# Kernel optimization log

Measured on AMD Instinct MI355X. Metric: run time of the kernel, lower is better.

Reference implementation:

```python
import jax, jax.numpy as jnp
import numpy as np

N_POINTS = 2_000_000
GRID = (128, 128, 128)
N_COMP = 3


def _bspline_weights(u):
    # cubic B-spline basis, returns tuple of 4 arrays shaped like u
    u2 = u * u
    u3 = u2 * u
    w0 = (1.0 - u) ** 3 / 6.0
    w1 = (3.0 * u3 - 6.0 * u2 + 4.0) / 6.0
    w2 = (-3.0 * u3 + 3.0 * u2 + 3.0 * u + 1.0) / 6.0
    w3 = u3 / 6.0
    return (w0, w1, w2, w3)


def setup_inputs() -> dict:
    key = jax.random.key(0)
    kx, ky, kz, kp = jax.random.split(key, 4)
    # query points uniform in the supported domain [-1, 1]
    x = jax.random.uniform(kx, (N_POINTS,), jnp.float32, -1.0, 1.0)
    y = jax.random.uniform(ky, (N_POINTS,), jnp.float32, -1.0, 1.0)
    z = jax.random.uniform(kz, (N_POINTS,), jnp.float32, -1.0, 1.0)
    phi_x = jax.random.normal(kp, (*GRID, N_COMP), jnp.float32)
    return {"x": x, "y": y, "z": z, "phi_x": phi_x}


def reference(x, y, z, phi_x):
    # BSplineField3d.vectorized_displacement with support_outside=True,
    # default support_range=None -> spacing = 2/(n-3), origin = -1 - spacing.
    nx, ny, nz, _ = phi_x.shape
    dx = 2.0 / (nx - 3)
    dy = 2.0 / (ny - 3)
    dz = 2.0 / (nz - 3)
    ox, oy, oz = -1.0 - dx, -1.0 - dy, -1.0 - dz

    u = (x - ox - dx) / dx
    v = (y - oy - dy) / dy
    w = (z - oz - dz) / dz
    ix = jnp.floor(u).astype(jnp.int32)
    iy = jnp.floor(v).astype(jnp.int32)
    iz = jnp.floor(w).astype(jnp.int32)
    u = u - ix
    v = v - iy
    w = w - iz

    wu = _bspline_weights(u)
    wv = _bspline_weights(v)
    ww = _bspline_weights(w)

    T = jnp.zeros((x.shape[0], phi_x.shape[-1]), dtype=x.dtype)
    # 64 fixed taps: gather from control grid at clamped indices, MAC.
    for l in range(4):
        ixl = jnp.clip(ix + l, 0, nx - 1)
        for m in range(4):
            iym = jnp.clip(iy + m, 0, ny - 1)
            wum = wu[l] * wv[m]
            for n in range(4):
                izn = jnp.clip(iz + n, 0, nz - 1)
                coef = wum * ww[n]  # [N]
                T = T + coef[:, None] * phi_x[ixl, iym, izn]  # gather [N, C]
    return T
```

## Files before the change

kernel.cpp:

```cpp
#include <hip/hip_runtime.h>


#define NBINS 4096
#define NBLK  256
#define BRICK 1331

__device__ __forceinline__ void bspline_w(float u, float& w0, float& w1,
                                          float& w2, float& w3) {
    const float u2 = u * u;
    const float u3 = u2 * u;
    const float t  = 1.0f - u;
    w0 = t * t * t * (1.0f / 6.0f);
    w1 = (3.0f * u3 - 6.0f * u2 + 4.0f) * (1.0f / 6.0f);
    w2 = (-3.0f * u3 + 3.0f * u2 + 3.0f * u + 1.0f) * (1.0f / 6.0f);
    w3 = u3 * (1.0f / 6.0f);
}

__device__ __forceinline__ void cell_ids(float x, float y, float z,
                                         int& ix, int& iy, int& iz) {
    const float dx = 2.0f / 125.0f;
    const float ox = -1.0f - dx;
    const float u = (x - ox - dx) / dx;
    const float v = (y - ox - dx) / dx;
    const float w = (z - ox - dx) / dx;
    ix = (int)floorf(u);
    iy = (int)floorf(v);
    iz = (int)floorf(w);
}

__device__ __forceinline__ int point_bin(float x, float y, float z) {
    int ix, iy, iz;
    cell_ids(x, y, z, ix, iy, iz);
    const int bx = min(max(ix, 0), 127) >> 3;
    const int by = min(max(iy, 0), 127) >> 3;
    const int bz = min(max(iz, 0), 127) >> 3;
    return (bx << 8) | (by << 4) | bz;
}

__global__ __launch_bounds__(256) void hist_kernel(
    const float* __restrict__ xs, const float* __restrict__ ys,
    const float* __restrict__ zs, unsigned* __restrict__ hist,
    int n, int chunk) {
    __shared__ unsigned h[NBINS];
    for (int j = threadIdx.x; j < NBINS; j += 256) h[j] = 0;
    __syncthreads();
    const int b = blockIdx.x;
    const int lo = b * chunk;
    const int hi = min(n, lo + chunk);
    for (int i = lo + threadIdx.x; i < hi; i += 256) {
        atomicAdd(&h[point_bin(xs[i], ys[i], zs[i])], 1u);
    }
    __syncthreads();
    for (int j = threadIdx.x; j < NBINS; j += 256) hist[b * NBINS + j] = h[j];
}

__global__ __launch_bounds__(256) void totals_kernel(
    const unsigned* __restrict__ hist, unsigned* __restrict__ total) {
    const int j = blockIdx.x * 256 + threadIdx.x;
    unsigned s = 0;
    for (int b = 0; b < NBLK; ++b) s += hist[b * NBINS + j];
    total[j] = s;
}

__global__ __launch_bounds__(1024) void scan_kernel(
    const unsigned* __restrict__ total, unsigned* __restrict__ binbase) {
    __shared__ unsigned sdata[1024];
    const int t = threadIdx.x;
    const unsigned v0 = total[4 * t + 0];
    const unsigned v1 = total[4 * t + 1];
    const unsigned v2 = total[4 * t + 2];
    const unsigned v3 = total[4 * t + 3];
    sdata[t] = v0 + v1 + v2 + v3;
    __syncthreads();
    for (int off = 1; off < 1024; off <<= 1) {
        unsigned x = (t >= off) ? sdata[t - off] : 0u;
        __syncthreads();
        sdata[t] += x;
        __syncthreads();
    }
    const unsigned ex = (t > 0) ? sdata[t - 1] : 0u;
    binbase[4 * t + 0] = ex;
    binbase[4 * t + 1] = ex + v0;
    binbase[4 * t + 2] = ex + v0 + v1;
    binbase[4 * t + 3] = ex + v0 + v1 + v2;
}

__global__ __launch_bounds__(256) void fixup_kernel(
    unsigned* __restrict__ hist, const unsigned* __restrict__ binbase) {
    const int j = blockIdx.x * 256 + threadIdx.x;
    unsigned run = binbase[j];
    for (int b = 0; b < NBLK; ++b) {
        const unsigned c = hist[b * NBINS + j];
        hist[b * NBINS + j] = run;
        run += c;
    }
}

__global__ __launch_bounds__(256) void scatter_kernel(
    const float* __restrict__ xs, const float* __restrict__ ys,
    const float* __restrict__ zs, const unsigned* __restrict__ hist,
    float4* __restrict__ rec, int n, int chunk) {
    __shared__ unsigned off[NBINS];
    const int b = blockIdx.x;
    for (int j = threadIdx.x; j < NBINS; j += 256) off[j] = hist[b * NBINS + j];
    __syncthreads();
    const int lo = b * chunk;
    const int hi = min(n, lo + chunk);
    for (int i = lo + threadIdx.x; i < hi; i += 256) {
        const float x = xs[i], y = ys[i], z = zs[i];
        const unsigned p = atomicAdd(&off[point_bin(x, y, z)], 1u);
        rec[p] = make_float4(x, y, z, __int_as_float(i));
    }
}

__global__ __launch_bounds__(256) void eval_kernel(
    const float4* __restrict__ rec, const unsigned* __restrict__ binbase,
    const unsigned* __restrict__ total, const float* __restrict__ phi,
    float* __restrict__ out) {
    const int bin = blockIdx.x;
    const unsigned cnt = total[bin];
    if (cnt == 0) return;
    const unsigned start = binbase[bin];

    const int gx0 = ((bin >> 8) & 15) << 3;
    const int gy0 = ((bin >> 4) & 15) << 3;
    const int gz0 = (bin & 15) << 3;

    __shared__ float4 brick[BRICK];
    for (int p = threadIdx.x; p < BRICK; p += 256) {
        const int lx = p / 121;
        const int r  = p - lx * 121;
        const int ly = r / 11;
        const int lz = r - ly * 11;
        const int gx = min(gx0 + lx, 127);
        const int gy = min(gy0 + ly, 127);
        const int gz = min(gz0 + lz, 127);
        const float* s = phi + (size_t)((gx * 128 + gy) * 128 + gz) * 3;
        brick[p] = make_float4(s[0], s[1], s[2], 0.0f);
    }
    __syncthreads();

    for (unsigned k = start + threadIdx.x; k < start + cnt; k += 256) {
        const float4 r4 = rec[k];
        const int idx = __float_as_int(r4.w);

        int ix, iy, iz;
        cell_ids(r4.x, r4.y, r4.z, ix, iy, iz);
        const float dx = 2.0f / 125.0f;
        const float ox = -1.0f - dx;
        float u = (r4.x - ox - dx) / dx - floorf((r4.x - ox - dx) / dx);
        float v = (r4.y - ox - dx) / dx - floorf((r4.y - ox - dx) / dx);
        float w = (r4.z - ox - dx) / dx - floorf((r4.z - ox - dx) / dx);

        float wu[4], wv[4], wz[4];
        bspline_w(u, wu[0], wu[1], wu[2], wu[3]);
        bspline_w(v, wv[0], wv[1], wv[2], wv[3]);
        bspline_w(w, wz[0], wz[1], wz[2], wz[3]);

        int izb = iz < 0 ? 0 : iz;
        const bool sh = izb > 124;
        if (sh) izb = 124;
        const float zw0 = sh ? 0.0f : wz[0];
        const float zw1 = sh ? wz[0] : wz[1];
        const float zw2 = sh ? wz[1] : wz[2];
        const float zw3 = sh ? (wz[2] + wz[3]) : wz[3];
        const int lzb = izb - gz0;

        int lxi[4], lyi[4];
#pragma unroll
        for (int l = 0; l < 4; ++l) {
            lxi[l] = min(max(ix + l, 0), 127) - gx0;
            lyi[l] = min(max(iy + l, 0), 127) - gy0;
        }

        float acc0 = 0.0f, acc1 = 0.0f, acc2 = 0.0f;
#pragma unroll
        for (int l = 0; l < 4; ++l) {
            const int rowx = lxi[l] * 11;
#pragma unroll
            for (int m = 0; m < 4; ++m) {
                const float4* p0 = &brick[(rowx + lyi[m]) * 11 + lzb];
                const float wm = wu[l] * wv[m];
                const float c0 = wm * zw0;
                const float c1 = wm * zw1;
                const float c2 = wm * zw2;
                const float c3 = wm * zw3;
                const float4 a = p0[0];
                const float4 b = p0[1];
                const float4 c = p0[2];
                const float d = c3;
                const float4 e = p0[3];
                acc0 = fmaf(c0, a.x, acc0);
                acc1 = fmaf(c0, a.y, acc1);
                acc2 = fmaf(c0, a.z, acc2);
                acc0 = fmaf(c1, b.x, acc0);
                acc1 = fmaf(c1, b.y, acc1);
                acc2 = fmaf(c1, b.z, acc2);
                acc0 = fmaf(c2, c.x, acc0);
                acc1 = fmaf(c2, c.y, acc1);
                acc2 = fmaf(c2, c.z, acc2);
                acc0 = fmaf(d, e.x, acc0);
                acc1 = fmaf(d, e.y, acc1);
                acc2 = fmaf(d, e.z, acc2);
            }
        }
        float* o = out + 3 * (size_t)idx;
        o[0] = acc0;
        o[1] = acc1;
        o[2] = acc2;
    }
}

__global__ __launch_bounds__(256) void bspline3d_direct(
    const float* __restrict__ xs, const float* __restrict__ ys,
    const float* __restrict__ zs, const float* __restrict__ phi,
    float* __restrict__ out, int n) {
    const int i = blockIdx.x * blockDim.x + threadIdx.x;
    if (i >= n) return;
    const float dx = 2.0f / 125.0f;
    const float ox = -1.0f - dx;
    float u = (xs[i] - ox - dx) / dx;
    float v = (ys[i] - ox - dx) / dx;
    float w = (zs[i] - ox - dx) / dx;
    const float fu = floorf(u), fv = floorf(v), fw = floorf(w);
    const int ix = (int)fu, iy = (int)fv, iz = (int)fw;
    u -= fu; v -= fv; w -= fw;
    float wu[4], wv[4], wz[4];
    bspline_w(u, wu[0], wu[1], wu[2], wu[3]);
    bspline_w(v, wv[0], wv[1], wv[2], wv[3]);
    bspline_w(w, wz[0], wz[1], wz[2], wz[3]);
    int izb = iz < 0 ? 0 : iz;
    const bool sh = izb > 124;
    if (sh) izb = 124;
    const float zw0 = sh ? 0.0f : wz[0];
    const float zw1 = sh ? wz[0] : wz[1];
    const float zw2 = sh ? wz[1] : wz[2];
    const float zw3 = sh ? (wz[2] + wz[3]) : wz[3];
    int xi[4], yi[4];
#pragma unroll
    for (int l = 0; l < 4; ++l) {
        xi[l] = min(max(ix + l, 0), 127);
        yi[l] = min(max(iy + l, 0), 127);
    }
    const float* pz = phi + izb * 3;
    float acc0 = 0.0f, acc1 = 0.0f, acc2 = 0.0f;
#pragma unroll
    for (int l = 0; l < 4; ++l) {
        const int rowx = xi[l] << 7;
#pragma unroll
        for (int m = 0; m < 4; ++m) {
            const float* p = pz + (rowx + yi[m]) * 384;
            const float4 a = *reinterpret_cast<const float4*>(p);
            const float4 b = *reinterpret_cast<const float4*>(p + 4);
            const float4 c = *reinterpret_cast<const float4*>(p + 8);
            const float wm = wu[l] * wv[m];
            const float c0 = wm * zw0, c1 = wm * zw1, c2 = wm * zw2, c3 = wm * zw3;
            acc0 = fmaf(c0, a.x, acc0); acc1 = fmaf(c0, a.y, acc1); acc2 = fmaf(c0, a.z, acc2);
            acc0 = fmaf(c1, a.w, acc0); acc1 = fmaf(c1, b.x, acc1); acc2 = fmaf(c1, b.y, acc2);
            acc0 = fmaf(c2, b.z, acc0); acc1 = fmaf(c2, b.w, acc1); acc2 = fmaf(c2, c.x, acc2);
            acc0 = fmaf(c3, c.y, acc0); acc1 = fmaf(c3, c.z, acc1); acc2 = fmaf(c3, c.w, acc2);
        }
    }
    float* o = out + 3 * (size_t)i;
    o[0] = acc0; o[1] = acc1; o[2] = acc2;
}

extern "C" void kernel_launch(void* const* d_in, const int* in_sizes, int n_in,
                              void* d_out, int out_size, void* d_ws,
                              size_t ws_size, hipStream_t stream) {
    const float* xs  = (const float*)d_in[0];
    const float* ys  = (const float*)d_in[1];
    const float* zs  = (const float*)d_in[2];
    const float* phi = (const float*)d_in[3];
    float* out = (float*)d_out;
    const int n = in_sizes[0];

    const size_t hist_off = 0;
    const size_t total_off = hist_off + (size_t)NBLK * NBINS * 4;
    const size_t base_off  = total_off + NBINS * 4;
    const size_t rec_off   = base_off + NBINS * 4;
    const size_t need = rec_off + (size_t)n * 16;

    if (ws_size < need) {
        const int block = 256;
        bspline3d_direct<<<(n + block - 1) / block, block, 0, stream>>>(
            xs, ys, zs, phi, out, n);
        return;
    }

    unsigned* hist    = (unsigned*)((char*)d_ws + hist_off);
    unsigned* total   = (unsigned*)((char*)d_ws + total_off);
    unsigned* binbase = (unsigned*)((char*)d_ws + base_off);
    float4*   rec     = (float4*)((char*)d_ws + rec_off);

    const int chunk = (n + NBLK - 1) / NBLK;

    hist_kernel<<<NBLK, 256, 0, stream>>>(xs, ys, zs, hist, n, chunk);
    totals_kernel<<<NBINS / 256, 256, 0, stream>>>(hist, total);
    scan_kernel<<<1, 1024, 0, stream>>>(total, binbase);
    fixup_kernel<<<NBINS / 256, 256, 0, stream>>>(hist, binbase);
    scatter_kernel<<<NBLK, 256, 0, stream>>>(xs, ys, zs, hist, rec, n, chunk);
    eval_kernel<<<NBINS, 256, 0, stream>>>(rec, binbase, total, phi, out);
}
```

Before: 234.3 us.

## Simplify binning with global atomics and repack shared brick as per-component z-windows

```diff
diff --git a/kernel.cpp b/kernel.cpp
--- a/kernel.cpp
+++ b/kernel.cpp
@@ -2,8 +2,8 @@
 
 
 #define NBINS 4096
-#define NBLK  256
-#define BRICK 1331
+#define CUR_STRIDE 16
+#define NW (121 * 8 * 3)
 
 __device__ __forceinline__ void bspline_w(float u, float& w0, float& w1,
                                           float& w2, float& w3) {
@@ -20,12 +20,9 @@
                                          int& ix, int& iy, int& iz) {
     const float dx = 2.0f / 125.0f;
     const float ox = -1.0f - dx;
-    const float u = (x - ox - dx) / dx;
-    const float v = (y - ox - dx) / dx;
-    const float w = (z - ox - dx) / dx;
-    ix = (int)floorf(u);
-    iy = (int)floorf(v);
-    iz = (int)floorf(w);
+    ix = (int)floorf((x - ox - dx) / dx);
+    iy = (int)floorf((y - ox - dx) / dx);
+    iz = (int)floorf((z - ox - dx) / dx);
 }
 
 __device__ __forceinline__ int point_bin(float x, float y, float z) {
@@ -39,37 +36,27 @@
 
 __global__ __launch_bounds__(256) void hist_kernel(
     const float* __restrict__ xs, const float* __restrict__ ys,
-    const float* __restrict__ zs, unsigned* __restrict__ hist,
-    int n, int chunk) {
+    const float* __restrict__ zs, unsigned* __restrict__ hist, int n) {
     __shared__ unsigned h[NBINS];
     for (int j = threadIdx.x; j < NBINS; j += 256) h[j] = 0;
     __syncthreads();
-    const int b = blockIdx.x;
-    const int lo = b * chunk;
-    const int hi = min(n, lo + chunk);
-    for (int i = lo + threadIdx.x; i < hi; i += 256) {
+    const int stride = gridDim.x * 256;
+    for (int i = blockIdx.x * 256 + threadIdx.x; i < n; i += stride)
         atomicAdd(&h[point_bin(xs[i], ys[i], zs[i])], 1u);
-    }
-    __syncthreads();
-    for (int j = threadIdx.x; j < NBINS; j += 256) hist[b * NBINS + j] = h[j];
-}
-
-__global__ __launch_bounds__(256) void totals_kernel(
-    const unsigned* __restrict__ hist, unsigned* __restrict__ total) {
-    const int j = blockIdx.x * 256 + threadIdx.x;
-    unsigned s = 0;
-    for (int b = 0; b < NBLK; ++b) s += hist[b * NBINS + j];
-    total[j] = s;
+    __syncthreads();
+    for (int j = threadIdx.x; j < NBINS; j += 256)
+        if (h[j]) atomicAdd(&hist[j], h[j]);
 }
 
 __global__ __launch_bounds__(1024) void scan_kernel(
-    const unsigned* __restrict__ total, unsigned* __restrict__ binbase) {
+    const unsigned* __restrict__ hist, unsigned* __restrict__ binbase,
+    unsigned* __restrict__ cursor) {
     __shared__ unsigned sdata[1024];
     const int t = threadIdx.x;
-    const unsigned v0 = total[4 * t + 0];
-    const unsigned v1 = total[4 * t + 1];
-    const unsigned v2 = total[4 * t + 2];
-    const unsigned v3 = total[4 * t + 3];
+    const unsigned v0 = hist[4 * t + 0];
+    const unsigned v1 = hist[4 * t + 1];
+    const unsigned v2 = hist[4 * t + 2];
+    const unsigned v3 = hist[4 * t + 3];
     sdata[t] = v0 + v1 + v2 + v3;
     __syncthreads();
     for (int off = 1; off < 1024; off <<= 1) {
@@ -79,46 +66,39 @@
         __syncthreads();
     }
     const unsigned ex = (t > 0) ? sdata[t - 1] : 0u;
-    binbase[4 * t + 0] = ex;
-    binbase[4 * t + 1] = ex + v0;
-    binbase[4 * t + 2] = ex + v0 + v1;
-    binbase[4 * t + 3] = ex + v0 + v1 + v2;
-}
-
-__global__ __launch_bounds__(256) void fixup_kernel(
-    unsigned* __restrict__ hist, const unsigned* __restrict__ binbase) {
-    const int j = blockIdx.x * 256 + threadIdx.x;
-    unsigned run = binbase[j];
-    for (int b = 0; b < NBLK; ++b) {
-        const unsigned c = hist[b * NBINS + j];
-        hist[b * NBINS + j] = run;
-        run += c;
-    }
+    const unsigned b0 = ex;
+    const unsigned b1 = ex + v0;
+    const unsigned b2 = b1 + v1;
+    const unsigned b3 = b2 + v2;
+    binbase[4 * t + 0] = b0;
+    binbase[4 * t + 1] = b1;
+    binbase[4 * t + 2] = b2;
+    binbase[4 * t + 3] = b3;
+    cursor[(4 * t + 0) * CUR_STRIDE] = b0;
+    cursor[(4 * t + 1) * CUR_STRIDE] = b1;
+    cursor[(4 * t + 2) * CUR_STRIDE] = b2;
+    cursor[(4 * t + 3) * CUR_STRIDE] = b3;
 }
 
 __global__ __launch_bounds__(256) void scatter_kernel(
     const float* __restrict__ xs, const float* __restrict__ ys,
-    const float* __restrict__ zs, const unsigned* __restrict__ hist,
-    float4* __restrict__ rec, int n, int chunk) {
-    __shared__ unsigned off[NBINS];
-    const int b = blockIdx.x;
-    for (int j = threadIdx.x; j < NBINS; j += 256) off[j] = hist[b * NBINS + j];
-    __syncthreads();
-    const int lo = b * chunk;
-    const int hi = min(n, lo + chunk);
-    for (int i = lo + threadIdx.x; i < hi; i += 256) {
+    const float* __restrict__ zs, unsigned* __restrict__ cursor,
+    float4* __restrict__ rec, int n) {
+    const int stride = gridDim.x * 256;
+    for (int i = blockIdx.x * 256 + threadIdx.x; i < n; i += stride) {
         const float x = xs[i], y = ys[i], z = zs[i];
-        const unsigned p = atomicAdd(&off[point_bin(x, y, z)], 1u);
+        const int bin = point_bin(x, y, z);
+        const unsigned p = atomicAdd(&cursor[bin * CUR_STRIDE], 1u);
         rec[p] = make_float4(x, y, z, __int_as_float(i));
     }
 }
 
 __global__ __launch_bounds__(256) void eval_kernel(
     const float4* __restrict__ rec, const unsigned* __restrict__ binbase,
-    const unsigned* __restrict__ total, const float* __restrict__ phi,
+    const unsigned* __restrict__ hist, const float* __restrict__ phi,
     float* __restrict__ out) {
     const int bin = blockIdx.x;
-    const unsigned cnt = total[bin];
+    const unsigned cnt = hist[bin];
     if (cnt == 0) return;
     const unsigned start = binbase[bin];
 
@@ -126,31 +106,39 @@
     const int gy0 = ((bin >> 4) & 15) << 3;
     const int gz0 = (bin & 15) << 3;
 
-    __shared__ float4 brick[BRICK];
-    for (int p = threadIdx.x; p < BRICK; p += 256) {
-        const int lx = p / 121;
-        const int r  = p - lx * 121;
-        const int ly = r / 11;
-        const int lz = r - ly * 11;
+    __shared__ float4 W[NW];
+    for (int p = threadIdx.x; p < NW; p += 256) {
+        const int c   = p % 3;
+        const int t   = p / 3;
+        const int s   = t & 7;
+        const int row = t >> 3;
+        const int lx  = row / 11;
+        const int ly  = row - lx * 11;
         const int gx = min(gx0 + lx, 127);
         const int gy = min(gy0 + ly, 127);
-        const int gz = min(gz0 + lz, 127);
-        const float* s = phi + (size_t)((gx * 128 + gy) * 128 + gz) * 3;
-        brick[p] = make_float4(s[0], s[1], s[2], 0.0f);
-    }
-    __syncthreads();
+        const float* src = phi + (size_t)((gx * 128 + gy) * 128) * 3 + c;
+        float4 v;
+        v.x = src[3 * min(gz0 + s + 0, 127)];
+        v.y = src[3 * min(gz0 + s + 1, 127)];
+        v.z = src[3 * min(gz0 + s + 2, 127)];
+        v.w = src[3 * min(gz0 + s + 3, 127)];
+        W[p] = v;
+    }
+    __syncthreads();
+
+    const float dx = 2.0f / 125.0f;
+    const float ox = -1.0f - dx;
 
     for (unsigned k = start + threadIdx.x; k < start + cnt; k += 256) {
         const float4 r4 = rec[k];
         const int idx = __float_as_int(r4.w);
 
-        int ix, iy, iz;
-        cell_ids(r4.x, r4.y, r4.z, ix, iy, iz);
-        const float dx = 2.0f / 125.0f;
-        const float ox = -1.0f - dx;
-        float u = (r4.x - ox - dx) / dx - floorf((r4.x - ox - dx) / dx);
-        float v = (r4.y - ox - dx) / dx - floorf((r4.y - ox - dx) / dx);
-        float w = (r4.z - ox - dx) / dx - floorf((r4.z - ox - dx) / dx);
+        const float U = (r4.x - ox - dx) / dx;
+        const float V = (r4.y - ox - dx) / dx;
+        const float Z = (r4.z - ox - dx) / dx;
+        const float fu = floorf(U), fv = floorf(V), fw = floorf(Z);
+        const int ix = (int)fu, iy = (int)fv, iz = (int)fw;
+        const float u = U - fu, v = V - fv, w = Z - fw;
 
         float wu[4], wv[4], wz[4];
         bspline_w(u, wu[0], wu[1], wu[2], wu[3]);
@@ -179,29 +167,27 @@
             const int rowx = lxi[l] * 11;
 #pragma unroll
             for (int m = 0; m < 4; ++m) {
-                const float4* p0 = &brick[(rowx + lyi[m]) * 11 + lzb];
+                const int base = ((rowx + lyi[m]) * 8 + lzb) * 3;
+                const float4 a = W[base + 0];
+                const float4 b = W[base + 1];
+                const float4 c = W[base + 2];
                 const float wm = wu[l] * wv[m];
                 const float c0 = wm * zw0;
                 const float c1 = wm * zw1;
                 const float c2 = wm * zw2;
                 const float c3 = wm * zw3;
-                const float4 a = p0[0];
-                const float4 b = p0[1];
-                const float4 c = p0[2];
-                const float d = c3;
-                const float4 e = p0[3];
                 acc0 = fmaf(c0, a.x, acc0);
-                acc1 = fmaf(c0, a.y, acc1);
-                acc2 = fmaf(c0, a.z, acc2);
-                acc0 = fmaf(c1, b.x, acc0);
+                acc0 = fmaf(c1, a.y, acc0);
+                acc0 = fmaf(c2, a.z, acc0);
+                acc0 = fmaf(c3, a.w, acc0);
+                acc1 = fmaf(c0, b.x, acc1);
                 acc1 = fmaf(c1, b.y, acc1);
-                acc2 = fmaf(c1, b.z, acc2);
-                acc0 = fmaf(c2, c.x, acc0);
-                acc1 = fmaf(c2, c.y, acc1);
+                acc1 = fmaf(c2, b.z, acc1);
+                acc1 = fmaf(c3, b.w, acc1);
+                acc2 = fmaf(c0, c.x, acc2);
+                acc2 = fmaf(c1, c.y, acc2);
                 acc2 = fmaf(c2, c.z, acc2);
-                acc0 = fmaf(d, e.x, acc0);
-                acc1 = fmaf(d, e.y, acc1);
-                acc2 = fmaf(d, e.z, acc2);
+                acc2 = fmaf(c3, c.w, acc2);
             }
         }
         float* o = out + 3 * (size_t)idx;
@@ -275,30 +261,26 @@
     float* out = (float*)d_out;
     const int n = in_sizes[0];
 
-    const size_t hist_off = 0;
-    const size_t total_off = hist_off + (size_t)NBLK * NBINS * 4;
-    const size_t base_off  = total_off + NBINS * 4;
-    const size_t rec_off   = base_off + NBINS * 4;
+    const size_t hist_off   = 0;
+    const size_t base_off   = hist_off + NBINS * 4;
+    const size_t cursor_off = base_off + NBINS * 4;
+    const size_t rec_off    = cursor_off + (size_t)NBINS * CUR_STRIDE * 4;
     const size_t need = rec_off + (size_t)n * 16;
 
     if (ws_size < need) {
-        const int block = 256;
-        bspline3d_direct<<<(n + block - 1) / block, block, 0, stream>>>(
-            xs, ys, zs, phi, out, n);
+        bspline3d_direct<<<(n + 255) / 256, 256, 0, stream>>>(xs, ys, zs, phi,
+                                                              out, n);
         return;
     }
 
     unsigned* hist    = (unsigned*)((char*)d_ws + hist_off);
-    unsigned* total   = (unsigned*)((char*)d_ws + total_off);
     unsigned* binbase = (unsigned*)((char*)d_ws + base_off);
+    unsigned* cursor  = (unsigned*)((char*)d_ws + cursor_off);
     float4*   rec     = (float4*)((char*)d_ws + rec_off);
 
-    const int chunk = (n + NBLK - 1) / NBLK;
-
-    hist_kernel<<<NBLK, 256, 0, stream>>>(xs, ys, zs, hist, n, chunk);
-    totals_kernel<<<NBINS / 256, 256, 0, stream>>>(hist, total);
-    scan_kernel<<<1, 1024, 0, stream>>>(total, binbase);
-    fixup_kernel<<<NBINS / 256, 256, 0, stream>>>(hist, binbase);
-    scatter_kernel<<<NBLK, 256, 0, stream>>>(xs, ys, zs, hist, rec, n, chunk);
-    eval_kernel<<<NBINS, 256, 0, stream>>>(rec, binbase, total, phi, out);
-}
+    hipMemsetAsync(hist, 0, NBINS * 4, stream);
+    hist_kernel<<<512, 256, 0, stream>>>(xs, ys, zs, hist, n);
+    scan_kernel<<<1, 1024, 0, stream>>>(hist, binbase, cursor);
+    scatter_kernel<<<512, 256, 0, stream>>>(xs, ys, zs, cursor, rec, n);
+    eval_kernel<<<NBINS, 256, 0, stream>>>(rec, binbase, hist, phi, out);
+}
```

Result: slower. 336.9 us (+43.8%).

## Merge column scan into totals, repack brick as z-quad float4s, widen eval blocks

Applied to the files above, without the earlier changes.

```diff
diff --git a/kernel.cpp b/kernel.cpp
--- a/kernel.cpp
+++ b/kernel.cpp
@@ -3,7 +3,6 @@
 
 #define NBINS 4096
 #define NBLK  256
-#define BRICK 1331
 
 __device__ __forceinline__ void bspline_w(float u, float& w0, float& w1,
                                           float& w2, float& w3) {
@@ -16,21 +15,12 @@
     w3 = u3 * (1.0f / 6.0f);
 }
 
-__device__ __forceinline__ void cell_ids(float x, float y, float z,
-                                         int& ix, int& iy, int& iz) {
+__device__ __forceinline__ int point_bin(float x, float y, float z) {
     const float dx = 2.0f / 125.0f;
     const float ox = -1.0f - dx;
-    const float u = (x - ox - dx) / dx;
-    const float v = (y - ox - dx) / dx;
-    const float w = (z - ox - dx) / dx;
-    ix = (int)floorf(u);
-    iy = (int)floorf(v);
-    iz = (int)floorf(w);
-}
-
-__device__ __forceinline__ int point_bin(float x, float y, float z) {
-    int ix, iy, iz;
-    cell_ids(x, y, z, ix, iy, iz);
+    const int ix = (int)floorf((x - ox - dx) / dx);
+    const int iy = (int)floorf((y - ox - dx) / dx);
+    const int iz = (int)floorf((z - ox - dx) / dx);
     const int bx = min(max(ix, 0), 127) >> 3;
     const int by = min(max(iy, 0), 127) >> 3;
     const int bz = min(max(iz, 0), 127) >> 3;
@@ -47,19 +37,23 @@
     const int b = blockIdx.x;
     const int lo = b * chunk;
     const int hi = min(n, lo + chunk);
-    for (int i = lo + threadIdx.x; i < hi; i += 256) {
+    for (int i = lo + threadIdx.x; i < hi; i += 256)
         atomicAdd(&h[point_bin(xs[i], ys[i], zs[i])], 1u);
-    }
     __syncthreads();
     for (int j = threadIdx.x; j < NBINS; j += 256) hist[b * NBINS + j] = h[j];
 }
 
-__global__ __launch_bounds__(256) void totals_kernel(
-    const unsigned* __restrict__ hist, unsigned* __restrict__ total) {
+__global__ __launch_bounds__(256) void colscan_kernel(
+    unsigned* __restrict__ hist, unsigned* __restrict__ total) {
     const int j = blockIdx.x * 256 + threadIdx.x;
-    unsigned s = 0;
-    for (int b = 0; b < NBLK; ++b) s += hist[b * NBINS + j];
-    total[j] = s;
+    unsigned run = 0;
+#pragma unroll 8
+    for (int b = 0; b < NBLK; ++b) {
+        const unsigned c = hist[b * NBINS + j];
+        hist[b * NBINS + j] = run;
+        run += c;
+    }
+    total[j] = run;
 }
 
 __global__ __launch_bounds__(1024) void scan_kernel(
@@ -85,24 +79,15 @@
     binbase[4 * t + 3] = ex + v0 + v1 + v2;
 }
 
-__global__ __launch_bounds__(256) void fixup_kernel(
-    unsigned* __restrict__ hist, const unsigned* __restrict__ binbase) {
-    const int j = blockIdx.x * 256 + threadIdx.x;
-    unsigned run = binbase[j];
-    for (int b = 0; b < NBLK; ++b) {
-        const unsigned c = hist[b * NBINS + j];
-        hist[b * NBINS + j] = run;
-        run += c;
-    }
-}
-
 __global__ __launch_bounds__(256) void scatter_kernel(
     const float* __restrict__ xs, const float* __restrict__ ys,
     const float* __restrict__ zs, const unsigned* __restrict__ hist,
-    float4* __restrict__ rec, int n, int chunk) {
+    const unsigned* __restrict__ binbase, float4* __restrict__ rec,
+    int n, int chunk) {
     __shared__ unsigned off[NBINS];
     const int b = blockIdx.x;
-    for (int j = threadIdx.x; j < NBINS; j += 256) off[j] = hist[b * NBINS + j];
+    for (int j = threadIdx.x; j < NBINS; j += 256)
+        off[j] = hist[b * NBINS + j] + binbase[j];
     __syncthreads();
     const int lo = b * chunk;
     const int hi = min(n, lo + chunk);
@@ -113,7 +98,7 @@
     }
 }
 
-__global__ __launch_bounds__(256) void eval_kernel(
+__global__ __launch_bounds__(512) void eval_kernel(
     const float4* __restrict__ rec, const unsigned* __restrict__ binbase,
     const unsigned* __restrict__ total, const float* __restrict__ phi,
     float* __restrict__ out) {
@@ -126,31 +111,60 @@
     const int gy0 = ((bin >> 4) & 15) << 3;
     const int gz0 = (bin & 15) << 3;
 
-    __shared__ float4 brick[BRICK];
-    for (int p = threadIdx.x; p < BRICK; p += 256) {
-        const int lx = p / 121;
-        const int r  = p - lx * 121;
-        const int ly = r / 11;
-        const int lz = r - ly * 11;
-        const int gx = min(gx0 + lx, 127);
-        const int gy = min(gy0 + ly, 127);
-        const int gz = min(gz0 + lz, 127);
-        const float* s = phi + (size_t)((gx * 128 + gy) * 128 + gz) * 3;
-        brick[p] = make_float4(s[0], s[1], s[2], 0.0f);
-    }
-    __syncthreads();
-
-    for (unsigned k = start + threadIdx.x; k < start + cnt; k += 256) {
+    __shared__ float raw[121 * 36];
+    __shared__ float4 W4[121 * 24];
+
+    if (gz0 <= 112) {
+        for (int p = threadIdx.x; p < 121 * 9; p += 512) {
+            const int row = p / 9;
+            const int q   = p - row * 9;
+            const int lx = row / 11, ly = row - (row / 11) * 11;
+            const int gx = min(gx0 + lx, 127);
+            const int gy = min(gy0 + ly, 127);
+            const float* src =
+                phi + (size_t)((gx * 128 + gy) * 128 + gz0) * 3 + q * 4;
+            *reinterpret_cast<float4*>(&raw[row * 36 + q * 4]) =
+                *reinterpret_cast<const float4*>(src);
+        }
+    } else {
+        for (int p = threadIdx.x; p < 121 * 11; p += 512) {
+            const int row = p / 11;
+            const int zz  = p - row * 11;
+            const int lx = row / 11, ly = row - (row / 11) * 11;
+            const int gx = min(gx0 + lx, 127);
+            const int gy = min(gy0 + ly, 127);
+            const int z  = min(gz0 + zz, 127);
+            const float* s = phi + (size_t)((gx * 128 + gy) * 128 + z) * 3;
+            raw[row * 36 + zz * 3 + 0] = s[0];
+            raw[row * 36 + zz * 3 + 1] = s[1];
+            raw[row * 36 + zz * 3 + 2] = s[2];
+        }
+    }
+    __syncthreads();
+
+    for (int p = threadIdx.x; p < 121 * 24; p += 512) {
+        const int row = p / 24;
+        const int t   = p - row * 24;
+        const int s   = t / 3;
+        const int c   = t - 3 * s;
+        const float* r = &raw[row * 36 + s * 3 + c];
+        W4[p] = make_float4(r[0], r[3], r[6], r[9]);
+    }
+    __syncthreads();
+
+    const float dx = 2.0f / 125.0f;
+    const float ox = -1.0f - dx;
+
+    for (unsigned k = start + threadIdx.x; k < start + cnt; k += 512) {
         const float4 r4 = rec[k];
         const int idx = __float_as_int(r4.w);
 
-        int ix, iy, iz;
-        cell_ids(r4.x, r4.y, r4.z, ix, iy, iz);
-        const float dx = 2.0f / 125.0f;
-        const float ox = -1.0f - dx;
-        float u = (r4.x - ox - dx) / dx - floorf((r4.x - ox - dx) / dx);
-        float v = (r4.y - ox - dx) / dx - floorf((r4.y - ox - dx) / dx);
-        float w = (r4.z - ox - dx) / dx - floorf((r4.z - ox - dx) / dx);
+        const float U = (r4.x - ox - dx) / dx;
+        const float V = (r4.y - ox - dx) / dx;
+        const float Z = (r4.z - ox - dx) / dx;
+        const float fu = floorf(U), fv = floorf(V), fw = floorf(Z);
+        const int ix = (int)fu, iy = (int)fv, iz = (int)fw;
+        const float u = U - fu, v = V - fv, w = Z - fw;
 
         float wu[4], wv[4], wz[4];
         bspline_w(u, wu[0], wu[1], wu[2], wu[3]);
@@ -164,7 +178,7 @@
         const float zw1 = sh ? wz[0] : wz[1];
         const float zw2 = sh ? wz[1] : wz[2];
         const float zw3 = sh ? (wz[2] + wz[3]) : wz[3];
-        const int lzb = izb - gz0;
+        const int lzb3 = (izb - gz0) * 3;
 
         int lxi[4], lyi[4];
 #pragma unroll
@@ -179,29 +193,27 @@
             const int rowx = lxi[l] * 11;
 #pragma unroll
             for (int m = 0; m < 4; ++m) {
-                const float4* p0 = &brick[(rowx + lyi[m]) * 11 + lzb];
+                const int base = (rowx + lyi[m]) * 24 + lzb3;
+                const float4 a  = W4[base + 0];
+                const float4 bb = W4[base + 1];
+                const float4 cc = W4[base + 2];
                 const float wm = wu[l] * wv[m];
                 const float c0 = wm * zw0;
                 const float c1 = wm * zw1;
                 const float c2 = wm * zw2;
                 const float c3 = wm * zw3;
-                const float4 a = p0[0];
-                const float4 b = p0[1];
-                const float4 c = p0[2];
-                const float d = c3;
-                const float4 e = p0[3];
                 acc0 = fmaf(c0, a.x, acc0);
-                acc1 = fmaf(c0, a.y, acc1);
-                acc2 = fmaf(c0, a.z, acc2);
-                acc0 = fmaf(c1, b.x, acc0);
-                acc1 = fmaf(c1, b.y, acc1);
-                acc2 = fmaf(c1, b.z, acc2);
-                acc0 = fmaf(c2, c.x, acc0);
-                acc1 = fmaf(c2, c.y, acc1);
-                acc2 = fmaf(c2, c.z, acc2);
-                acc0 = fmaf(d, e.x, acc0);
-                acc1 = fmaf(d, e.y, acc1);
-                acc2 = fmaf(d, e.z, acc2);
+                acc0 = fmaf(c1, a.y, acc0);
+                acc0 = fmaf(c2, a.z, acc0);
+                acc0 = fmaf(c3, a.w, acc0);
+                acc1 = fmaf(c0, bb.x, acc1);
+                acc1 = fmaf(c1, bb.y, acc1);
+                acc1 = fmaf(c2, bb.z, acc1);
+                acc1 = fmaf(c3, bb.w, acc1);
+                acc2 = fmaf(c0, cc.x, acc2);
+                acc2 = fmaf(c1, cc.y, acc2);
+                acc2 = fmaf(c2, cc.z, acc2);
+                acc2 = fmaf(c3, cc.w, acc2);
             }
         }
         float* o = out + 3 * (size_t)idx;
@@ -275,16 +287,15 @@
     float* out = (float*)d_out;
     const int n = in_sizes[0];
 
-    const size_t hist_off = 0;
+    const size_t hist_off  = 0;
     const size_t total_off = hist_off + (size_t)NBLK * NBINS * 4;
     const size_t base_off  = total_off + NBINS * 4;
     const size_t rec_off   = base_off + NBINS * 4;
     const size_t need = rec_off + (size_t)n * 16;
 
     if (ws_size < need) {
-        const int block = 256;
-        bspline3d_direct<<<(n + block - 1) / block, block, 0, stream>>>(
-            xs, ys, zs, phi, out, n);
+        bspline3d_direct<<<(n + 255) / 256, 256, 0, stream>>>(xs, ys, zs, phi,
+                                                              out, n);
         return;
     }
 
@@ -296,9 +307,9 @@
     const int chunk = (n + NBLK - 1) / NBLK;
 
     hist_kernel<<<NBLK, 256, 0, stream>>>(xs, ys, zs, hist, n, chunk);
-    totals_kernel<<<NBINS / 256, 256, 0, stream>>>(hist, total);
+    colscan_kernel<<<NBINS / 256, 256, 0, stream>>>(hist, total);
     scan_kernel<<<1, 1024, 0, stream>>>(total, binbase);
-    fixup_kernel<<<NBINS / 256, 256, 0, stream>>>(hist, binbase);
-    scatter_kernel<<<NBLK, 256, 0, stream>>>(xs, ys, zs, hist, rec, n, chunk);
-    eval_kernel<<<NBINS, 256, 0, stream>>>(rec, binbase, total, phi, out);
-}
+    scatter_kernel<<<NBLK, 256, 0, stream>>>(xs, ys, zs, hist, binbase, rec, n,
+                                             chunk);
+    eval_kernel<<<NBINS, 512, 0, stream>>>(rec, binbase, total, phi, out);
+}
```

Measured after the change: 224.7 us. 4.1% less time.
